# Kernel tuning notes

Measured on AMD Instinct MI355X. Metric: run time of the kernel, lower is better.

Reference implementation:

```python
import jax, jax.numpy as jnp
import numpy as np

B, T, C = 2, 2048, 2048
H, KV, DH = 32, 8, 64
GROUP = H // KV  # 4


def _rope_tables(seq_len, half_dim):
    # standard RoPE frequencies: theta_i = 10000^(-2i/d)
    inv_freq = 1.0 / (10000.0 ** (np.arange(half_dim, dtype=np.float32) * 2.0 / (2 * half_dim)))
    ang = np.arange(seq_len, dtype=np.float32)[:, None] * inv_freq[None, :]  # [T, D/2]
    return jnp.asarray(np.sin(ang)), jnp.asarray(np.cos(ang))


def setup_inputs() -> dict:
    key = jax.random.key(0)
    ks = jax.random.split(key, 5)
    scale = 0.02
    sin, cos = _rope_tables(T, DH // 2)
    return {
        "x": jax.random.normal(ks[0], (B, T, C), jnp.float32),
        "Wq": jax.random.normal(ks[1], (C, H * DH), jnp.float32) * scale,
        "Wk": jax.random.normal(ks[2], (C, KV * DH), jnp.float32) * scale,
        "Wv": jax.random.normal(ks[3], (C, KV * DH), jnp.float32) * scale,
        "Wout": jax.random.normal(ks[4], (H * DH, C), jnp.float32) * scale,
        "rope_sin": sin,
        "rope_cos": cos,
        "swa_window": 2048,
    }


def apply_rope(x, sin, cos):
    # x: [B, T, Hh, D]; interleaved-pair rotation, computed in fp32
    b, t, h, d = x.shape
    orig_dtype = x.dtype
    xf = x.astype(jnp.float32).reshape(b, t, h, d // 2, 2)
    x1, x2 = xf[..., 0], xf[..., 1]
    s = sin[:t].astype(jnp.float32)[None, :, None, :]  # [1,T,1,D/2]
    c = cos[:t].astype(jnp.float32)[None, :, None, :]
    o1 = x1 * c - x2 * s
    o2 = x1 * s + x2 * c
    return jnp.stack([o1, o2], axis=-1).reshape(b, t, h, d).astype(orig_dtype)


def reference(x, Wq, Wk, Wv, Wout, rope_sin, rope_cos, swa_window):
    b, t, c = x.shape
    q = (x @ Wq).reshape(b, t, H, DH)
    k = (x @ Wk).reshape(b, t, KV, DH)
    v = (x @ Wv).reshape(b, t, KV, DH)
    q = apply_rope(q, rope_sin, rope_cos)
    k = apply_rope(k, rope_sin, rope_cos)
    # expand KV heads (repeat_interleave along head dim)
    k_e = jnp.repeat(k, GROUP, axis=2)  # [B,T,H,DH]
    v_e = jnp.repeat(v, GROUP, axis=2)
    scale = 1.0 / jnp.sqrt(jnp.float32(DH))
    scores = jnp.einsum('bqhd,bkhd->bhqk', q, k_e) * scale  # [B,H,T,T]
    idx = jnp.arange(t)
    causal_mask = idx[None, :] > idx[:, None]                 # j > i
    older = (idx[:, None] - idx[None, :]) > swa_window        # beyond window
    mask = causal_mask | older
    scores = jnp.where(mask[None, None], -jnp.inf, scores)
    weights = jax.nn.softmax(scores, axis=-1)
    attn = jnp.einsum('bhqk,bkhd->bqhd', weights, v_e).reshape(b, t, c)
    return attn @ Wout
```

## Files before the change

### kernel.cpp

```cpp
#include <hip/hip_runtime.h>

typedef unsigned short u16;
typedef unsigned int u32;
typedef __attribute__((ext_vector_type(8))) short bf16x8;
typedef __attribute__((ext_vector_type(4))) float f32x4;

#define B_   2
#define T_   2048
#define C_   2048
#define H_   32
#define KVH_ 8
#define DH_  64
#define QKVS 3072
#define KOFF 2048
#define VOFF 2560

__device__ __forceinline__ u16 f2bf(float f) {
  union { float f; unsigned u; } v; v.f = f;
  unsigned r = (v.u + 0x7fffu + ((v.u >> 16) & 1u)) >> 16;
  return (u16)r;
}
__device__ __forceinline__ float bf2f(u16 u) {
  union { unsigned u; float f; } v; v.u = ((unsigned)u) << 16;
  return v.f;
}
__device__ __forceinline__ void async_copy16(void* lds, const void* g) {
  __builtin_amdgcn_global_load_lds((const __attribute__((address_space(1))) void*)g,
                                   (__attribute__((address_space(3))) void*)lds, 16, 0, 0);
}

__global__ void cvt_bf16_kernel(const float* __restrict__ in, u16* __restrict__ out, int n4) {
  int i = blockIdx.x * 256 + threadIdx.x;
  if (i >= n4) return;
  const float4 v = reinterpret_cast<const float4*>(in)[i];
  union { u16 h[4]; unsigned long long ll; } o;
  o.h[0] = f2bf(v.x); o.h[1] = f2bf(v.y); o.h[2] = f2bf(v.z); o.h[3] = f2bf(v.w);
  reinterpret_cast<unsigned long long*>(out)[i] = o.ll;
}

__global__ void transpose_w_kernel(const float* __restrict__ W, u16* __restrict__ Wt,
                                   int K_, int N_) {
  __shared__ float tile[32][33];
  int n0 = blockIdx.x * 32, k0 = blockIdx.y * 32;
  int tx = threadIdx.x, ty = threadIdx.y;
#pragma unroll
  for (int i = 0; i < 4; i++)
    tile[ty + i * 8][tx] = W[(long)(k0 + ty + i * 8) * N_ + n0 + tx];
  __syncthreads();
#pragma unroll
  for (int i = 0; i < 4; i++)
    Wt[(long)(n0 + ty + i * 8) * K_ + k0 + tx] = f2bf(tile[tx][ty + i * 8]);
}

__global__ void rope_kernel(u16* __restrict__ buf, const float* __restrict__ sT,
                            const float* __restrict__ cT, int rowstride, int ncols) {
  int row = blockIdx.y;
  int c4 = (blockIdx.x * 128 + threadIdx.x) * 4;
  if (c4 >= ncols) return;
  int t = row & (T_ - 1);
  int pair = (c4 & (DH_ - 1)) >> 1;
  u16* p = buf + (long)row * rowstride + c4;
  union { u16 h[4]; unsigned long long ll; } v;
  v.ll = *reinterpret_cast<unsigned long long*>(p);
  float x0 = bf2f(v.h[0]), x1 = bf2f(v.h[1]), x2 = bf2f(v.h[2]), x3 = bf2f(v.h[3]);
  float s0 = sT[t * 32 + pair],     c0 = cT[t * 32 + pair];
  float s1 = sT[t * 32 + pair + 1], c1 = cT[t * 32 + pair + 1];
  v.h[0] = f2bf(x0 * c0 - x1 * s0);
  v.h[1] = f2bf(x0 * s0 + x1 * c0);
  v.h[2] = f2bf(x2 * c1 - x3 * s1);
  v.h[3] = f2bf(x2 * s1 + x3 * c1);
  *reinterpret_cast<unsigned long long*>(p) = v.ll;
}

template <int OUT_F32>
__global__ __launch_bounds__(256, 3) void gemm_nt(const u16* __restrict__ A,
                                                  const u16* __restrict__ Bt,
                                                  void* __restrict__ Cout,
                                                  int M_, int N_, int K_) {
  __shared__ alignas(16) u16 As[128 * 32];
  __shared__ alignas(16) u16 Bs[128 * 32];
  const int t = threadIdx.x;
  const int w = t >> 6, l = t & 63;
  const int m0 = blockIdx.y * 128, n0 = blockIdx.x * 128;
  const int wr = (w >> 1) * 64, wc = (w & 1) * 64;
  const int lr = l & 15, lk = (l >> 4) * 8;

  f32x4 acc[4][4];
#pragma unroll
  for (int i = 0; i < 4; i++)
#pragma unroll
    for (int j = 0; j < 4; j++) {
      f32x4 z = {0.f, 0.f, 0.f, 0.f};
      acc[i][j] = z;
    }

  const int arow = t >> 2, acol = (t & 3) * 8;
  const u16* Ag = A + (long)(m0 + arow) * K_ + acol;
  const u16* Bg = Bt + (long)(n0 + arow) * K_ + acol;
  char* AsB = (char*)As;
  char* BsB = (char*)Bs;
  const int ldsbase = (w << 10);

  for (int kt = 0; kt < K_; kt += 32) {
    async_copy16(AsB + ldsbase, Ag + kt);
    async_copy16(AsB + 4096 + ldsbase, Ag + (long)64 * K_ + kt);
    async_copy16(BsB + ldsbase, Bg + kt);
    async_copy16(BsB + 4096 + ldsbase, Bg + (long)64 * K_ + kt);
    __syncthreads();
    bf16x8 a[4], b[4];
#pragma unroll
    for (int i = 0; i < 4; i++) a[i] = *(const bf16x8*)(As + (wr + i * 16 + lr) * 32 + lk);
#pragma unroll
    for (int i = 0; i < 4; i++) b[i] = *(const bf16x8*)(Bs + (wc + i * 16 + lr) * 32 + lk);
#pragma unroll
    for (int i = 0; i < 4; i++)
#pragma unroll
      for (int j = 0; j < 4; j++)
        acc[i][j] = __builtin_amdgcn_mfma_f32_16x16x32_bf16(a[i], b[j], acc[i][j], 0, 0, 0);
    __syncthreads();
  }

  const int lg = l >> 4;
#pragma unroll
  for (int i = 0; i < 4; i++)
#pragma unroll
    for (int j = 0; j < 4; j++)
#pragma unroll
      for (int r = 0; r < 4; r++) {
        long row = m0 + wr + i * 16 + lg * 4 + r;
        long col = n0 + wc + j * 16 + lr;
        float v = acc[i][j][r];
        if (OUT_F32)
          ((float*)Cout)[row * N_ + col] = v;
        else
          ((u16*)Cout)[row * N_ + col] = f2bf(v);
      }
}

__global__ __launch_bounds__(256, 3) void attn_fwd(const u16* __restrict__ qkv,
                                                   u16* __restrict__ o,
                                                   const int* __restrict__ swa_ptr) {
  __shared__ alignas(16) u16 Klds[64 * 64];
  __shared__ alignas(16) u16 VTlds[64 * 64];
  __shared__ alignas(16) u16 Plds[4][16 * 64];
  const int t = threadIdx.x, w = t >> 6, l = t & 63;
  const int b = blockIdx.z, h = blockIdx.y, bx = blockIdx.x;
  const int kvh = h >> 2;
  const int swa = *swa_ptr;
  const int lr = l & 15, lg = l >> 4;
  const int swz = (lr & 7) << 4;
  const int sbase = (l & 48) | (lg << 2);
  char* myP = (char*)Plds + w * 2048;

  const int krow = t >> 3, kch = t & 7;
  const int kvp = (t & 31) * 2, dch = (t >> 5) * 8;

  for (int pass = 0; pass < 2; pass++) {
    const int qtile = pass ? (31 - bx) : bx;
    const int q0 = qtile * 64;

    bf16x8 qa[2];
    const long qrow = (long)(b * T_ + q0 + w * 16 + lr);
#pragma unroll
    for (int kk = 0; kk < 2; kk++)
      qa[kk] = *(const bf16x8*)(qkv + qrow * QKVS + h * 64 + kk * 32 + lg * 8);

    f32x4 ofrag[4];
#pragma unroll
    for (int nf = 0; nf < 4; nf++) {
      f32x4 z = {0.f, 0.f, 0.f, 0.f};
      ofrag[nf] = z;
    }
    float mrun = -1e30f, srun = 0.f;

    const int lo = q0 - swa - 63;
    const int startt = lo > 0 ? ((lo + 63) >> 6) : 0;

    bf16x8 K0, K1, V0, V1;
    {
      const u16* kbase = qkv + (long)(b * T_ + startt * 64) * QKVS + KOFF + kvh * 64;
      K0 = *(const bf16x8*)(kbase + (long)krow * QKVS + kch * 8);
      K1 = *(const bf16x8*)(kbase + (long)(krow + 32) * QKVS + kch * 8);
      const u16* vbase = qkv + (long)(b * T_ + startt * 64) * QKVS + VOFF + kvh * 64 + dch;
      V0 = *(const bf16x8*)(vbase + (long)kvp * QKVS);
      V1 = *(const bf16x8*)(vbase + (long)(kvp + 1) * QKVS);
    }

    for (int tt = startt; tt <= qtile; tt++) {
      const int kv0 = tt * 64;
      __syncthreads();
      *(bf16x8*)((char*)Klds + ((krow * 128 + kch * 16) ^ ((krow & 7) << 4))) = K0;
      *(bf16x8*)((char*)Klds + (((krow + 32) * 128 + kch * 16) ^ ((krow & 7) << 4))) = K1;
#pragma unroll
      for (int i = 0; i < 8; i++) {
        int d = dch + i;
        int off = (d * 128 + kvp * 2) ^ ((d & 7) << 4);
        u32 pack = ((u32)(u16)V0[i]) | (((u32)(u16)V1[i]) << 16);
        *(u32*)((char*)VTlds + off) = pack;
      }
      __syncthreads();
      if (tt < qtile) {
        const u16* kbase = qkv + (long)(b * T_ + kv0 + 64) * QKVS + KOFF + kvh * 64;
        K0 = *(const bf16x8*)(kbase + (long)krow * QKVS + kch * 8);
        K1 = *(const bf16x8*)(kbase + (long)(krow + 32) * QKVS + kch * 8);
        const u16* vbase = qkv + (long)(b * T_ + kv0 + 64) * QKVS + VOFF + kvh * 64 + dch;
        V0 = *(const bf16x8*)(vbase + (long)kvp * QKVS);
        V1 = *(const bf16x8*)(vbase + (long)(kvp + 1) * QKVS);
      }

      f32x4 s[4];
#pragma unroll
      for (int nf = 0; nf < 4; nf++) {
        f32x4 acc = {0.f, 0.f, 0.f, 0.f};
#pragma unroll
        for (int kk = 0; kk < 2; kk++) {
          int koff = ((nf * 16 + lr) * 128 + (kk * 32 + lg * 8) * 2) ^ swz;
          bf16x8 kb = *(const bf16x8*)((char*)Klds + koff);
          acc = __builtin_amdgcn_mfma_f32_16x16x32_bf16(kb, qa[kk], acc, 0, 0, 0);
        }
        s[nf] = acc;
      }

      const int i_abs = q0 + w * 16 + lr;
      float pm = -3e38f;
#pragma unroll
      for (int nf = 0; nf < 4; nf++)
#pragma unroll
        for (int r = 0; r < 4; r++) {
          int j = kv0 + nf * 16 + lg * 4 + r;
          float sv = s[nf][r] * 0.125f;
          bool ok = (j <= i_abs) && (i_abs - j <= swa);
          sv = ok ? sv : -3e38f;
          s[nf][r] = sv;
          pm = fmaxf(pm, sv);
        }
      pm = fmaxf(pm, __shfl_xor(pm, 16));
      pm = fmaxf(pm, __shfl_xor(pm, 32));

      float mnew = fmaxf(mrun, pm);
      float fac = __expf(mrun - mnew);
      mrun = mnew;
      float rs = 0.f;
#pragma unroll
      for (int nf = 0; nf < 4; nf++)
#pragma unroll
        for (int r = 0; r < 4; r++) {
          float p = __expf(s[nf][r] - mrun);
          s[nf][r] = p;
          rs += p;
        }
      rs += __shfl_xor(rs, 16);
      rs += __shfl_xor(rs, 32);
      srun = srun * fac + rs;

#pragma unroll
      for (int nf = 0; nf < 4; nf++) {
        u32 lo32 = ((u32)f2bf(s[nf][0])) | (((u32)f2bf(s[nf][1])) << 16);
        u32 hi32 = ((u32)f2bf(s[nf][2])) | (((u32)f2bf(s[nf][3])) << 16);
        unsigned long long pk = ((unsigned long long)hi32 << 32) | lo32;
        int off = (lr * 128 + nf * 32 + lg * 8) ^ swz;
        *(unsigned long long*)(myP + off) = pk;
      }

      float facr[4];
#pragma unroll
      for (int r = 0; r < 4; r++) facr[r] = __shfl(fac, sbase + r);
#pragma unroll
      for (int nf = 0; nf < 4; nf++)
#pragma unroll
        for (int r = 0; r < 4; r++) ofrag[nf][r] *= facr[r];

      asm volatile("s_waitcnt lgkmcnt(0)" ::: "memory");
      bf16x8 pa[2];
#pragma unroll
      for (int kk = 0; kk < 2; kk++) {
        int poff = (lr * 128 + kk * 64 + lg * 16) ^ swz;
        pa[kk] = *(const bf16x8*)(myP + poff);
      }
#pragma unroll
      for (int nf = 0; nf < 4; nf++)
#pragma unroll
        for (int kk = 0; kk < 2; kk++) {
          int voff = ((nf * 16 + lr) * 128 + (kk * 32 + lg * 8) * 2) ^ swz;
          bf16x8 vb = *(const bf16x8*)((char*)VTlds + voff);
          ofrag[nf] = __builtin_amdgcn_mfma_f32_16x16x32_bf16(pa[kk], vb, ofrag[nf], 0, 0, 0);
        }
    }

    float inv = 1.0f / srun;
    float invr[4];
#pragma unroll
    for (int r = 0; r < 4; r++) invr[r] = __shfl(inv, sbase + r);
    const long orow = (long)(b * T_ + q0 + w * 16);
#pragma unroll
    for (int nf = 0; nf < 4; nf++)
#pragma unroll
      for (int r = 0; r < 4; r++)
        o[(orow + lg * 4 + r) * 2048 + h * 64 + nf * 16 + lr] = f2bf(ofrag[nf][r] * invr[r]);
  }
}

extern "C" void kernel_launch(void* const* d_in, const int* in_sizes, int n_in,
                              void* d_out, int out_size, void* d_ws, size_t ws_size,
                              hipStream_t stream) {
  const float* x    = (const float*)d_in[0];
  const float* Wq   = (const float*)d_in[1];
  const float* Wk   = (const float*)d_in[2];
  const float* Wv   = (const float*)d_in[3];
  const float* Wout = (const float*)d_in[4];
  const float* rsin = (const float*)d_in[5];
  const float* rcos = (const float*)d_in[6];
  const int*   swa  = (const int*)d_in[7];
  float* out = (float*)d_out;

  char* ws = (char*)d_ws;
  u16* xb    = (u16*)(ws);
  u16* ab    = xb;
  u16* wqkvT = (u16*)(ws + 16777216);
  u16* woT   = wqkvT;
  u16* qkvb  = (u16*)(ws + 29360128);

  cvt_bf16_kernel<<<dim3(8192), dim3(256), 0, stream>>>(x, xb, 2097152);
  transpose_w_kernel<<<dim3(64, 64), dim3(32, 8), 0, stream>>>(Wq, wqkvT, 2048, 2048);
  transpose_w_kernel<<<dim3(16, 64), dim3(32, 8), 0, stream>>>(Wk, wqkvT + (long)2048 * 2048, 2048, 512);
  transpose_w_kernel<<<dim3(16, 64), dim3(32, 8), 0, stream>>>(Wv, wqkvT + (long)2560 * 2048, 2048, 512);

  gemm_nt<0><<<dim3(24, 32), dim3(256), 0, stream>>>(xb, wqkvT, qkvb, 4096, 3072, 2048);

  transpose_w_kernel<<<dim3(64, 64), dim3(32, 8), 0, stream>>>(Wout, woT, 2048, 2048);

  rope_kernel<<<dim3(5, 4096), dim3(128), 0, stream>>>(qkvb, rsin, rcos, QKVS, 2560);

  attn_fwd<<<dim3(16, 32, 2), dim3(256), 0, stream>>>(qkvb, ab, swa);

  gemm_nt<1><<<dim3(16, 32), dim3(256), 0, stream>>>(ab, woT, out, 4096, 2048, 2048);
}
```

Baseline: 340.3 us.

## Fold softmax scale into RoPE, use exp2, skip interior masking, remap workgroups

The RoPE kernel now multiplies the Q columns by 0.125*log2(e), so the attention kernel can use exp2f and drop the per-score scale multiply. The mask loop is skipped for tiles that lie entirely inside the causal window. P is packed to bf16 with the hardware v_cvt_pk_bf16_f32 instruction instead of software rounding. Workgroup indices in both the GEMM and the attention kernel are remapped to spread neighbouring blocks across the XCDs, which could change cache locality.

```diff
diff --git a/kernel.cpp b/kernel.cpp
--- a/kernel.cpp
+++ b/kernel.cpp
@@ -24,6 +24,11 @@
   union { unsigned u; float f; } v; v.u = ((unsigned)u) << 16;
   return v.f;
 }
+__device__ __forceinline__ u32 cvt_pk_bf16(float lo, float hi) {
+  u32 r;
+  asm("v_cvt_pk_bf16_f32 %0, %1, %2" : "=v"(r) : "v"(lo), "v"(hi));
+  return r;
+}
 __device__ __forceinline__ void async_copy16(void* lds, const void* g) {
   __builtin_amdgcn_global_load_lds((const __attribute__((address_space(1))) void*)g,
                                    (__attribute__((address_space(3))) void*)lds, 16, 0, 0);
@@ -57,14 +62,15 @@
   int row = blockIdx.y;
   int c4 = (blockIdx.x * 128 + threadIdx.x) * 4;
   if (c4 >= ncols) return;
+  const float S = (blockIdx.x < 4) ? 0.18033688f : 1.0f;
   int t = row & (T_ - 1);
   int pair = (c4 & (DH_ - 1)) >> 1;
   u16* p = buf + (long)row * rowstride + c4;
   union { u16 h[4]; unsigned long long ll; } v;
   v.ll = *reinterpret_cast<unsigned long long*>(p);
   float x0 = bf2f(v.h[0]), x1 = bf2f(v.h[1]), x2 = bf2f(v.h[2]), x3 = bf2f(v.h[3]);
-  float s0 = sT[t * 32 + pair],     c0 = cT[t * 32 + pair];
-  float s1 = sT[t * 32 + pair + 1], c1 = cT[t * 32 + pair + 1];
+  float s0 = sT[t * 32 + pair] * S,     c0 = cT[t * 32 + pair] * S;
+  float s1 = sT[t * 32 + pair + 1] * S, c1 = cT[t * 32 + pair + 1] * S;
   v.h[0] = f2bf(x0 * c0 - x1 * s0);
   v.h[1] = f2bf(x0 * s0 + x1 * c0);
   v.h[2] = f2bf(x2 * c1 - x3 * s1);
@@ -81,7 +87,11 @@
   __shared__ alignas(16) u16 Bs[128 * 32];
   const int t = threadIdx.x;
   const int w = t >> 6, l = t & 63;
-  const int m0 = blockIdx.y * 128, n0 = blockIdx.x * 128;
+  const int gx = gridDim.x;
+  const int nwg = gx * gridDim.y;
+  const int flat = blockIdx.y * gx + blockIdx.x;
+  const int f2 = (flat & 7) * (nwg >> 3) + (flat >> 3);
+  const int m0 = (f2 / gx) * 128, n0 = (f2 % gx) * 128;
   const int wr = (w >> 1) * 64, wc = (w & 1) * 64;
   const int lr = l & 15, lk = (l >> 4) * 8;
 
@@ -144,7 +154,9 @@
   __shared__ alignas(16) u16 VTlds[64 * 64];
   __shared__ alignas(16) u16 Plds[4][16 * 64];
   const int t = threadIdx.x, w = t >> 6, l = t & 63;
-  const int b = blockIdx.z, h = blockIdx.y, bx = blockIdx.x;
+  const int flat = blockIdx.x + (blockIdx.y << 4) + (blockIdx.z << 9);
+  const int f2 = (flat & 7) * 128 + (flat >> 3);
+  const int bx = f2 & 15, h = (f2 >> 4) & 31, b = f2 >> 9;
   const int kvh = h >> 2;
   const int swa = *swa_ptr;
   const int lr = l & 15, lg = l >> 4;
@@ -222,30 +234,37 @@
       }
 
       const int i_abs = q0 + w * 16 + lr;
+      const int wmin = q0 + w * 16;
       float pm = -3e38f;
-#pragma unroll
-      for (int nf = 0; nf < 4; nf++)
-#pragma unroll
-        for (int r = 0; r < 4; r++) {
-          int j = kv0 + nf * 16 + lg * 4 + r;
-          float sv = s[nf][r] * 0.125f;
-          bool ok = (j <= i_abs) && (i_abs - j <= swa);
-          sv = ok ? sv : -3e38f;
-          s[nf][r] = sv;
-          pm = fmaxf(pm, sv);
-        }
+      if ((kv0 + 63 > wmin) || (wmin + 15 - kv0 > swa)) {
+#pragma unroll
+        for (int nf = 0; nf < 4; nf++)
+#pragma unroll
+          for (int r = 0; r < 4; r++) {
+            int j = kv0 + nf * 16 + lg * 4 + r;
+            bool ok = (j <= i_abs) && (i_abs - j <= swa);
+            float sv = ok ? s[nf][r] : -3e38f;
+            s[nf][r] = sv;
+            pm = fmaxf(pm, sv);
+          }
+      } else {
+#pragma unroll
+        for (int nf = 0; nf < 4; nf++)
+#pragma unroll
+          for (int r = 0; r < 4; r++) pm = fmaxf(pm, s[nf][r]);
+      }
       pm = fmaxf(pm, __shfl_xor(pm, 16));
       pm = fmaxf(pm, __shfl_xor(pm, 32));
 
       float mnew = fmaxf(mrun, pm);
-      float fac = __expf(mrun - mnew);
+      float fac = exp2f(mrun - mnew);
       mrun = mnew;
       float rs = 0.f;
 #pragma unroll
       for (int nf = 0; nf < 4; nf++)
 #pragma unroll
         for (int r = 0; r < 4; r++) {
-          float p = __expf(s[nf][r] - mrun);
+          float p = exp2f(s[nf][r] - mrun);
           s[nf][r] = p;
           rs += p;
         }
@@ -255,8 +274,8 @@
 
 #pragma unroll
       for (int nf = 0; nf < 4; nf++) {
-        u32 lo32 = ((u32)f2bf(s[nf][0])) | (((u32)f2bf(s[nf][1])) << 16);
-        u32 hi32 = ((u32)f2bf(s[nf][2])) | (((u32)f2bf(s[nf][3])) << 16);
+        u32 lo32 = cvt_pk_bf16(s[nf][0], s[nf][1]);
+        u32 hi32 = cvt_pk_bf16(s[nf][2], s[nf][3]);
         unsigned long long pk = ((unsigned long long)hi32 << 32) | lo32;
         int off = (lr * 128 + nf * 32 + lg * 8) ^ swz;
         *(unsigned long long*)(myP + off) = pk;
```

Measured after the change: 333.4 us. 2.0% less time.
